# Optimization experiments

Measured on AMD Instinct MI355X. Metric: run time of the kernel, lower is better.

Reference implementation:

```python
import jax, jax.numpy as jnp
import numpy as np

B, S, D_IN, H, L = 32, 1024, 128, 256, 2
ND = 2  # bidirectional


def setup_inputs() -> dict:
    key = jax.random.key(0)
    ks = iter(jax.random.split(key, 40))

    def p(shape, scale=0.05):
        return jax.random.normal(next(ks), shape, dtype=jnp.float32) * scale

    inp = {"x": jax.random.normal(next(ks), (B, S, D_IN), dtype=jnp.float32)}
    dims_in = [D_IN, H * ND]
    for l in range(L):
        for tag in ("f", "b"):
            inp[f"w_ih_l{l}{tag}"] = p((4 * H, dims_in[l]))
            inp[f"w_hh_l{l}{tag}"] = p((4 * H, H))
            inp[f"b_l{l}{tag}"] = p((4 * H,))  # b_ih + b_hh fused (identical math)
    inp["attn_w"] = p((H * ND,))   # nn.Linear(2H, 1) weight
    inp["attn_b"] = p((1,))
    inp["head_w"] = p((D_IN, H * ND))  # forecasting head: Linear(2H, input_dim)
    inp["head_b"] = p((D_IN,))
    return inp


def _lstm_dir(x, w_ih, w_hh, b, reverse):
    """Single-direction LSTM over [B,S,F] -> [B,S,H]. PyTorch gate order i,f,g,o."""
    Bb = x.shape[0]
    Hh = w_hh.shape[1]
    # Precompute input projections once: [S,B,4H]
    xp = jnp.einsum('bsi,gi->sbg', x, w_ih) + b
    if reverse:
        xp = xp[::-1]
    h0 = jnp.zeros((Bb, Hh), x.dtype)
    c0 = jnp.zeros((Bb, Hh), x.dtype)

    def step(carry, gx):
        h, c = carry
        g = gx + h @ w_hh.T
        i, f, gg, o = jnp.split(g, 4, axis=-1)
        c = jax.nn.sigmoid(f) * c + jax.nn.sigmoid(i) * jnp.tanh(gg)
        h = jax.nn.sigmoid(o) * jnp.tanh(c)
        return (h, c), h

    _, hs = jax.lax.scan(step, (h0, c0), xp)
    if reverse:
        hs = hs[::-1]
    return jnp.swapaxes(hs, 0, 1)  # [B,S,H]


def reference(x,
              w_ih_l0f, w_hh_l0f, b_l0f, w_ih_l0b, w_hh_l0b, b_l0b,
              w_ih_l1f, w_hh_l1f, b_l1f, w_ih_l1b, w_hh_l1b, b_l1b,
              attn_w, attn_b, head_w, head_b):
    h = x
    layers = [((w_ih_l0f, w_hh_l0f, b_l0f), (w_ih_l0b, w_hh_l0b, b_l0b)),
              ((w_ih_l1f, w_hh_l1f, b_l1f), (w_ih_l1b, w_hh_l1b, b_l1b))]
    for fw, bw in layers:
        hf = _lstm_dir(h, *fw, False)
        hb = _lstm_dir(h, *bw, True)
        h = jnp.concatenate([hf, hb], axis=-1)  # [B,S,2H]; dropout off (eval)
    # Prefix attention pooling: original recomputes softmax over output[:, :i+1]
    # for every i. Equivalently (softmax is shift-invariant per prefix):
    # context_i = cumsum(e * h)_i / cumsum(e)_i with e = exp(s - max(s)).
    s = h @ attn_w + attn_b[0]                      # [B,S] attention scores
    e = jnp.exp(s - jnp.max(s, axis=1, keepdims=True))
    num = jnp.cumsum(e[..., None] * h, axis=1)      # [B,S,2H]
    den = jnp.cumsum(e, axis=1)[..., None]          # [B,S,1]
    context = num / den                             # [B,S,2H]
    forecasts = context @ head_w.T + head_b         # [B,S,D_IN]
    return forecasts
```

## Files before the change

### kernel.cpp

```cpp
#include <hip/hip_runtime.h>

typedef unsigned short ushort_t;
typedef unsigned int uint_t;
typedef unsigned long long u64;
typedef __attribute__((ext_vector_type(8))) short short8;
typedef __attribute__((ext_vector_type(4))) float floatx4;

#define S_LEN 1024
#define BATCH 32
#define HDIM  256
#define GDIM  1024
#define DIN   128
#define SALT  0x00C0FFEE00000000ULL

__device__ __forceinline__ float bf2f(ushort_t u) { return __uint_as_float(((unsigned)u) << 16); }
__device__ __forceinline__ float bf2fs(short s)   { return __uint_as_float(((unsigned)(unsigned short)s) << 16); }
__device__ __forceinline__ ushort_t f2bf(float f) {
  unsigned u = __float_as_uint(f);
  unsigned r = (u + 0x7fffu + ((u >> 16) & 1u)) >> 16;
  return (ushort_t)r;
}
__device__ __forceinline__ float sigf(float x) { return 1.f / (1.f + __expf(-x)); }
__device__ __forceinline__ float tanh_f(float x) {
  float ax = fabsf(x);
  float e = __expf(2.f * ax);
  float r = 1.f - 2.f / (e + 1.f);
  return x < 0.f ? -r : r;
}

__device__ __forceinline__ void load_lds16(const void* g, void* l) {
  __builtin_amdgcn_global_load_lds((const __attribute__((address_space(1))) unsigned int*)g,
                                   (__attribute__((address_space(3))) unsigned int*)l, 16, 0, 0);
}
__device__ __forceinline__ void vm0() { asm volatile("s_waitcnt vmcnt(0)" ::: "memory"); }

__global__ __launch_bounds__(256) void gemm_bf16(
    const ushort_t* __restrict__ A, const ushort_t* __restrict__ Bw,
    const float* __restrict__ bias, void* __restrict__ Cout,
    int M, int N, int K, int mode)
{
  __shared__ __align__(16) ushort_t As[128 * 64];
  __shared__ __align__(16) ushort_t Bs[128 * 64];
  const int tid = threadIdx.x;
  const int lane = tid & 63, wid = tid >> 6;
  const int wm = wid >> 1, wn = wid & 1;
  const int bm = blockIdx.y, bn = blockIdx.x;
  const int l15 = lane & 15, q4 = lane >> 4;

  const int r  = tid >> 3;
  const int c8 = tid & 7;
  const int g8 = c8 ^ (r & 7);

  floatx4 zero4 = {0.f, 0.f, 0.f, 0.f};
  floatx4 acc[4][4];
#pragma unroll
  for (int mt = 0; mt < 4; ++mt)
#pragma unroll
    for (int nt = 0; nt < 4; ++nt) acc[mt][nt] = zero4;

  for (int k0 = 0; k0 < K; k0 += 64) {
    __syncthreads();
#pragma unroll
    for (int p = 0; p < 4; ++p) {
      int row = p * 32 + r;
      load_lds16(A + (size_t)(bm * 128 + row) * K + k0 + g8 * 8, (void*)(As + p * 2048 + wid * 512));
      load_lds16(Bw + (size_t)(bn * 128 + row) * K + k0 + g8 * 8, (void*)(Bs + p * 2048 + wid * 512));
    }
    __syncthreads();
#pragma unroll
    for (int ks = 0; ks < 2; ++ks) {
      const int kk = ks * 4 + q4;
      short8 af[4], bf[4];
#pragma unroll
      for (int mt = 0; mt < 4; ++mt) {
        int row = wm * 64 + mt * 16 + l15;
        af[mt] = *(const short8*)(As + row * 64 + ((kk ^ (row & 7)) << 3));
      }
#pragma unroll
      for (int nt = 0; nt < 4; ++nt) {
        int row = wn * 64 + nt * 16 + l15;
        bf[nt] = *(const short8*)(Bs + row * 64 + ((kk ^ (row & 7)) << 3));
      }
#pragma unroll
      for (int mt = 0; mt < 4; ++mt)
#pragma unroll
        for (int nt = 0; nt < 4; ++nt)
          acc[mt][nt] = __builtin_amdgcn_mfma_f32_16x16x32_bf16(af[mt], bf[nt], acc[mt][nt], 0, 0, 0);
    }
  }

#pragma unroll
  for (int mt = 0; mt < 4; ++mt)
#pragma unroll
    for (int nt = 0; nt < 4; ++nt)
#pragma unroll
      for (int rr = 0; rr < 4; ++rr) {
        int m = bm * 128 + wm * 64 + mt * 16 + q4 * 4 + rr;
        int n = bn * 128 + wn * 64 + nt * 16 + l15;
        float v = acc[mt][nt][rr] + bias[n];
        if (mode == 0) {
          ((ushort_t*)Cout)[(size_t)m * N + n] = f2bf(v);
        } else if (mode == 1) {
          int t = m >> 5, b = m & 31;
          ((float*)Cout)[(size_t)b * (S_LEN * DIN) + t * DIN + n] = v;
        } else {
          int t = m >> 5, b = m & 31;
          ((ushort_t*)Cout)[(size_t)t * (N * 32) + n * 32 + b] = f2bf(v);
        }
      }
}

__global__ __launch_bounds__(256) void lstm_layer(
    const ushort_t* __restrict__ xpf, const ushort_t* __restrict__ xpb,
    const ushort_t* __restrict__ whhf, const ushort_t* __restrict__ whhb,
    ushort_t* __restrict__ hout, u64* __restrict__ comm, u64* __restrict__ epochs)
{
  const int bx = blockIdx.x;
  const int dir = bx & 1, j = bx >> 1;

  const ushort_t* xp  = dir ? xpb : xpf;
  const ushort_t* whh = dir ? whhb : whhf;
  u64* commd = comm + (size_t)dir * 4096;
  const int hoff = dir * 256;

  __shared__ __align__(16) ushort_t hbuf[32 * 264];
  __shared__ __align__(16) float stage[32 * 132];

  const int tid = threadIdx.x, lane = tid & 63, w = tid >> 6;
  const int l15 = lane & 15, q4 = lane >> 4;

  short8 Bf[2][8];
#pragma unroll
  for (int tl = 0; tl < 2; ++tl) {
    int grow = w * 256 + j * 32 + tl * 16 + l15;
#pragma unroll
    for (int ks = 0; ks < 8; ++ks)
      Bf[tl][ks] = *(const short8*)(whh + (size_t)grow * 256 + ks * 32 + q4 * 8);
  }

  for (int i = tid; i < 32 * 132; i += 256) ((uint_t*)hbuf)[i] = 0u;

  float cst[4] = {0.f, 0.f, 0.f, 0.f};

  u64 xr64[2][2];
  auto ldxp = [&](int tt) {
#pragma unroll
    for (int mt = 0; mt < 2; ++mt)
#pragma unroll
      for (int tl = 0; tl < 2; ++tl) {
        int g = w * 256 + j * 32 + tl * 16 + l15;
        xr64[mt][tl] = *(const u64*)(xp + (size_t)tt * (GDIM * BATCH) + (size_t)g * 32 + mt * 16 + q4 * 4);
      }
  };

  const int cb  = tid >> 3;
  const int cg0 = tid & 7;
  const int bb  = tid >> 3;
  const int c4  = (tid & 7) * 4;

  ldxp((dir == 0) ? 0 : 1023);
  __syncthreads();

  for (int sc = 0; sc < 1024; ++sc) {
    const int tcur  = (dir == 0) ? sc : 1023 - sc;
    const int tnext = (dir == 0) ? (sc < 1023 ? sc + 1 : 1023) : (sc < 1023 ? 1022 - sc : 0);

    floatx4 acc[2][2];
#pragma unroll
    for (int mt = 0; mt < 2; ++mt)
#pragma unroll
      for (int tl = 0; tl < 2; ++tl) {
        u64 v = xr64[mt][tl];
#pragma unroll
        for (int rr = 0; rr < 4; ++rr)
          acc[mt][tl][rr] = bf2f((ushort_t)(v >> (16 * rr)));
      }

    ldxp(tnext);

    if (sc > 0) {
      if (w == 0) {
        const u64 want = SALT | (u64)(unsigned)sc;
        const u64* ea = epochs + ((size_t)(dir * 2 + (sc & 1)) * 8 + (lane & 7)) * 16;
        for (;;) {
          u64 v = __hip_atomic_load(ea, __ATOMIC_RELAXED, __HIP_MEMORY_SCOPE_AGENT);
          if (__ballot(v == want) == ~0ULL) break;
        }
      }
      __syncthreads();
      const u64* rbuf = commd + (size_t)(sc & 1) * 2048 + (size_t)cb * 64 + cg0 * 8;
      u64 tmp[8];
#pragma unroll
      for (int k = 0; k < 8; ++k)
        tmp[k] = __hip_atomic_load(rbuf + k, __ATOMIC_RELAXED, __HIP_MEMORY_SCOPE_AGENT);
#pragma unroll
      for (int k = 0; k < 8; ++k)
        *(u64*)(hbuf + cb * 264 + cg0 * 32 + k * 4) = tmp[k];
    }
    __syncthreads();

#pragma unroll
    for (int ks = 0; ks < 8; ++ks) {
      short8 a0 = *(const short8*)(hbuf + l15 * 264 + ks * 32 + q4 * 8);
      short8 a1 = *(const short8*)(hbuf + (16 + l15) * 264 + ks * 32 + q4 * 8);
      acc[0][0] = __builtin_amdgcn_mfma_f32_16x16x32_bf16(a0, Bf[0][ks], acc[0][0], 0, 0, 0);
      acc[0][1] = __builtin_amdgcn_mfma_f32_16x16x32_bf16(a0, Bf[1][ks], acc[0][1], 0, 0, 0);
      acc[1][0] = __builtin_amdgcn_mfma_f32_16x16x32_bf16(a1, Bf[0][ks], acc[1][0], 0, 0, 0);
      acc[1][1] = __builtin_amdgcn_mfma_f32_16x16x32_bf16(a1, Bf[1][ks], acc[1][1], 0, 0, 0);
    }

#pragma unroll
    for (int mt = 0; mt < 2; ++mt)
#pragma unroll
      for (int tl = 0; tl < 2; ++tl)
#pragma unroll
        for (int rr = 0; rr < 4; ++rr)
          stage[(mt * 16 + q4 * 4 + rr) * 132 + w * 32 + tl * 16 + l15] = acc[mt][tl][rr];
    __syncthreads();

    float hv4[4];
#pragma unroll
    for (int i = 0; i < 4; ++i) {
      float gi = stage[bb * 132 +       c4 + i];
      float gf = stage[bb * 132 + 32  + c4 + i];
      float gg = stage[bb * 132 + 64  + c4 + i];
      float go = stage[bb * 132 + 96  + c4 + i];
      float c = sigf(gf) * cst[i] + sigf(gi) * tanh_f(gg);
      cst[i] = c;
      hv4[i] = sigf(go) * tanh_f(c);
    }
    u64 pv = (u64)f2bf(hv4[0]) | ((u64)f2bf(hv4[1]) << 16) |
             ((u64)f2bf(hv4[2]) << 32) | ((u64)f2bf(hv4[3]) << 48);

    __hip_atomic_store(commd + (size_t)((sc + 1) & 1) * 2048 + (size_t)bb * 64 + j * 8 + (tid & 7),
                       pv, __ATOMIC_RELAXED, __HIP_MEMORY_SCOPE_AGENT);
    *(u64*)(hout + (size_t)tcur * (BATCH * 512) + bb * 512 + hoff + j * 32 + c4) = pv;
    vm0();
    __syncthreads();
    if (tid == 0)
      __hip_atomic_store(epochs + ((size_t)(dir * 2 + ((sc + 1) & 1)) * 8 + j) * 16,
                         SALT | (u64)(unsigned)(sc + 1), __ATOMIC_RELAXED, __HIP_MEMORY_SCOPE_AGENT);
  }
}

__global__ __launch_bounds__(256) void attn_scores(
    const ushort_t* __restrict__ h1, const float* __restrict__ attn_w,
    const float* __restrict__ attn_b, float* __restrict__ e_out)
{
  const int b = blockIdx.x;
  __shared__ float sbuf[1024];
  __shared__ float red[4];
  const int tid = threadIdx.x, lane = tid & 63, w = tid >> 6;

  float wreg[8];
#pragma unroll
  for (int i = 0; i < 8; ++i) wreg[i] = attn_w[lane * 8 + i];

  for (int t = w; t < 1024; t += 4) {
    short8 hv = *(const short8*)(h1 + (size_t)t * (BATCH * 512) + b * 512 + lane * 8);
    float dot = 0.f;
#pragma unroll
    for (int i = 0; i < 8; ++i) dot += bf2fs(hv[i]) * wreg[i];
#pragma unroll
    for (int off = 32; off; off >>= 1) dot += __shfl_xor(dot, off);
    if (lane == 0) sbuf[t] = dot + attn_b[0];
  }
  __syncthreads();
  float m = -1e30f;
  for (int t = tid; t < 1024; t += 256) m = fmaxf(m, sbuf[t]);
#pragma unroll
  for (int off = 32; off; off >>= 1) m = fmaxf(m, __shfl_xor(m, off));
  if (lane == 0) red[w] = m;
  __syncthreads();
  float mm = fmaxf(fmaxf(red[0], red[1]), fmaxf(red[2], red[3]));
  for (int t = tid; t < 1024; t += 256) e_out[b * 1024 + t] = __expf(sbuf[t] - mm);
}

__global__ __launch_bounds__(256) void attn_ctx(
    const ushort_t* __restrict__ h1, const float* __restrict__ e_in, ushort_t* __restrict__ ctx)
{
  const int b = blockIdx.x >> 1, half = blockIdx.x & 1;
  const int c = half * 256 + threadIdx.x;
  float num = 0.f, den = 0.f;
  const ushort_t* hp = h1 + b * 512 + c;
  ushort_t* cp = ctx + b * 512 + c;
  const float* ep = e_in + b * 1024;
#pragma unroll 4
  for (int t = 0; t < 1024; ++t) {
    float ev = ep[t];
    float hv = bf2f(hp[(size_t)t * (BATCH * 512)]);
    num += ev * hv;
    den += ev;
    cp[(size_t)t * (BATCH * 512)] = f2bf(num / den);
  }
}

__global__ void castw(const float* __restrict__ in, ushort_t* __restrict__ out, int n) {
  int i = blockIdx.x * 256 + threadIdx.x;
  if (i < n) out[i] = f2bf(in[i]);
}
__global__ void castx(const float* __restrict__ x, ushort_t* __restrict__ xt) {
  int i = blockIdx.x * 256 + threadIdx.x;
  int dcol = i & 127;
  int m = i >> 7;
  int b = m & 31, s = m >> 5;
  xt[i] = f2bf(x[(size_t)b * (S_LEN * DIN) + s * DIN + dcol]);
}

extern "C" void kernel_launch(void* const* d_in, const int* in_sizes, int n_in,
                              void* d_out, int out_size, void* d_ws, size_t ws_size,
                              hipStream_t stream)
{
  const float* x     = (const float*)d_in[0];
  const float* wih0f = (const float*)d_in[1];
  const float* whh0f = (const float*)d_in[2];
  const float* b0f   = (const float*)d_in[3];
  const float* wih0b = (const float*)d_in[4];
  const float* whh0b = (const float*)d_in[5];
  const float* b0b   = (const float*)d_in[6];
  const float* wih1f = (const float*)d_in[7];
  const float* whh1f = (const float*)d_in[8];
  const float* b1f   = (const float*)d_in[9];
  const float* wih1b = (const float*)d_in[10];
  const float* whh1b = (const float*)d_in[11];
  const float* b1b   = (const float*)d_in[12];
  const float* attw  = (const float*)d_in[13];
  const float* attb  = (const float*)d_in[14];
  const float* headw = (const float*)d_in[15];
  const float* headb = (const float*)d_in[16];
  float* out = (float*)d_out;

  char* p = (char*)d_ws;
  auto alloc = [&](size_t bytes) {
    char* r = p;
    p += (bytes + 511) & ~(size_t)511;
    return r;
  };
  u64* ep0        = (u64*)alloc(512 * 8);
  u64* ep1        = (u64*)alloc(512 * 8);
  u64* comm0      = (u64*)alloc(8192 * 8);
  u64* comm1      = (u64*)alloc(8192 * 8);
  ushort_t* xt    = (ushort_t*)alloc((size_t)32768 * 128 * 2);
  ushort_t* cwih0f = (ushort_t*)alloc(131072 * 2);
  ushort_t* cwih0b = (ushort_t*)alloc(131072 * 2);
  ushort_t* cwhh0f = (ushort_t*)alloc(262144 * 2);
  ushort_t* cwhh0b = (ushort_t*)alloc(262144 * 2);
  ushort_t* cwih1f = (ushort_t*)alloc(524288 * 2);
  ushort_t* cwih1b = (ushort_t*)alloc(524288 * 2);
  ushort_t* cwhh1f = (ushort_t*)alloc(262144 * 2);
  ushort_t* cwhh1b = (ushort_t*)alloc(262144 * 2);
  ushort_t* cwhead = (ushort_t*)alloc(65536 * 2);
  ushort_t* xpA = (ushort_t*)alloc((size_t)32768 * 1024 * 2);
  ushort_t* xpB = (ushort_t*)alloc((size_t)32768 * 1024 * 2);
  ushort_t* h0  = (ushort_t*)alloc((size_t)32768 * 512 * 2);
  ushort_t* h1  = (ushort_t*)alloc((size_t)32768 * 512 * 2);
  float* ebuf   = (float*)alloc(32 * 1024 * 4);
  ushort_t* ctx = xpA;

  (void)in_sizes; (void)n_in; (void)out_size; (void)ws_size;

  (void)hipMemsetAsync(ep0, 0, 2 * 512 * 8, stream);

  castw<<<512, 256, 0, stream>>>(wih0f, cwih0f, 131072);
  castw<<<512, 256, 0, stream>>>(wih0b, cwih0b, 131072);
  castw<<<1024, 256, 0, stream>>>(whh0f, cwhh0f, 262144);
  castw<<<1024, 256, 0, stream>>>(whh0b, cwhh0b, 262144);
  castw<<<2048, 256, 0, stream>>>(wih1f, cwih1f, 524288);
  castw<<<2048, 256, 0, stream>>>(wih1b, cwih1b, 524288);
  castw<<<1024, 256, 0, stream>>>(whh1f, cwhh1f, 262144);
  castw<<<1024, 256, 0, stream>>>(whh1b, cwhh1b, 262144);
  castw<<<256, 256, 0, stream>>>(headw, cwhead, 65536);
  castx<<<16384, 256, 0, stream>>>(x, xt);

  gemm_bf16<<<dim3(8, 256), 256, 0, stream>>>(xt, cwih0f, b0f, xpA, 32768, 1024, 128, 2);
  gemm_bf16<<<dim3(8, 256), 256, 0, stream>>>(xt, cwih0b, b0b, xpB, 32768, 1024, 128, 2);
  lstm_layer<<<16, 256, 0, stream>>>(xpA, xpB, cwhh0f, cwhh0b, h0, comm0, ep0);

  gemm_bf16<<<dim3(8, 256), 256, 0, stream>>>(h0, cwih1f, b1f, xpA, 32768, 1024, 512, 2);
  gemm_bf16<<<dim3(8, 256), 256, 0, stream>>>(h0, cwih1b, b1b, xpB, 32768, 1024, 512, 2);
  lstm_layer<<<16, 256, 0, stream>>>(xpA, xpB, cwhh1f, cwhh1b, h1, comm1, ep1);

  attn_scores<<<32, 256, 0, stream>>>(h1, attw, attb, ebuf);
  attn_ctx<<<64, 256, 0, stream>>>(h1, ebuf, ctx);
  gemm_bf16<<<dim3(1, 256), 256, 0, stream>>>(ctx, cwhead, headb, out, 32768, 128, 512, 1);
}
```

Baseline: 7.826 ms.

## Replace epoch flags with per-element tagged hidden-state exchange in LSTM recurrence

```diff
diff --git a/kernel.cpp b/kernel.cpp
--- a/kernel.cpp
+++ b/kernel.cpp
@@ -11,7 +11,6 @@
 #define HDIM  256
 #define GDIM  1024
 #define DIN   128
-#define SALT  0x00C0FFEE00000000ULL
 
 __device__ __forceinline__ float bf2f(ushort_t u) { return __uint_as_float(((unsigned)u) << 16); }
 __device__ __forceinline__ float bf2fs(short s)   { return __uint_as_float(((unsigned)(unsigned short)s) << 16); }
@@ -32,7 +31,6 @@
   __builtin_amdgcn_global_load_lds((const __attribute__((address_space(1))) unsigned int*)g,
                                    (__attribute__((address_space(3))) unsigned int*)l, 16, 0, 0);
 }
-__device__ __forceinline__ void vm0() { asm volatile("s_waitcnt vmcnt(0)" ::: "memory"); }
 
 __global__ __launch_bounds__(256) void gemm_bf16(
     const ushort_t* __restrict__ A, const ushort_t* __restrict__ Bw,
@@ -113,18 +111,18 @@
 __global__ __launch_bounds__(256) void lstm_layer(
     const ushort_t* __restrict__ xpf, const ushort_t* __restrict__ xpb,
     const ushort_t* __restrict__ whhf, const ushort_t* __restrict__ whhb,
-    ushort_t* __restrict__ hout, u64* __restrict__ comm, u64* __restrict__ epochs)
+    ushort_t* __restrict__ hout, uint_t* __restrict__ comm)
 {
   const int bx = blockIdx.x;
   const int dir = bx & 1, j = bx >> 1;
 
   const ushort_t* xp  = dir ? xpb : xpf;
   const ushort_t* whh = dir ? whhb : whhf;
-  u64* commd = comm + (size_t)dir * 4096;
+  uint_t* commd = comm + (size_t)dir * 16384;
   const int hoff = dir * 256;
 
   __shared__ __align__(16) ushort_t hbuf[32 * 264];
-  __shared__ __align__(16) float stage[32 * 132];
+  __shared__ __align__(16) float stage[32 * 133];
 
   const int tid = threadIdx.x, lane = tid & 63, w = tid >> 6;
   const int l15 = lane & 15, q4 = lane >> 4;
@@ -155,7 +153,6 @@
 
   const int cb  = tid >> 3;
   const int cg0 = tid & 7;
-  const int bb  = tid >> 3;
   const int c4  = (tid & 7) * 4;
 
   ldxp((dir == 0) ? 0 : 1023);
@@ -178,24 +175,29 @@
 
     ldxp(tnext);
 
-    if (sc > 0) {
-      if (w == 0) {
-        const u64 want = SALT | (u64)(unsigned)sc;
-        const u64* ea = epochs + ((size_t)(dir * 2 + (sc & 1)) * 8 + (lane & 7)) * 16;
-        for (;;) {
-          u64 v = __hip_atomic_load(ea, __ATOMIC_RELAXED, __HIP_MEMORY_SCOPE_AGENT);
-          if (__ballot(v == want) == ~0ULL) break;
+    if (sc > 0 && cg0 != j) {
+      const u64* rbuf = (const u64*)(commd + (size_t)(sc & 1) * 8192 + cb * 256 + cg0 * 32);
+      const uint_t want = (uint_t)sc;
+      u64 wv[16];
+      for (;;) {
+        uint_t bad = 0;
+#pragma unroll
+        for (int k = 0; k < 16; ++k)
+          wv[k] = __hip_atomic_load(rbuf + k, __ATOMIC_RELAXED, __HIP_MEMORY_SCOPE_AGENT);
+#pragma unroll
+        for (int k = 0; k < 16; ++k) {
+          bad |= ((uint_t)wv[k] ^ want);
+          bad |= ((uint_t)(wv[k] >> 32) ^ want);
         }
-      }
-      __syncthreads();
-      const u64* rbuf = commd + (size_t)(sc & 1) * 2048 + (size_t)cb * 64 + cg0 * 8;
-      u64 tmp[8];
-#pragma unroll
-      for (int k = 0; k < 8; ++k)
-        tmp[k] = __hip_atomic_load(rbuf + k, __ATOMIC_RELAXED, __HIP_MEMORY_SCOPE_AGENT);
-#pragma unroll
-      for (int k = 0; k < 8; ++k)
-        *(u64*)(hbuf + cb * 264 + cg0 * 32 + k * 4) = tmp[k];
+        if (!(bad & 0xFFFFu)) break;
+      }
+#pragma unroll
+      for (int k = 0; k < 8; ++k) {
+        u64 a = wv[2 * k], b = wv[2 * k + 1];
+        uint_t p01 = (((uint_t)(a >> 16)) & 0xFFFFu) | (((uint_t)(a >> 32)) & 0xFFFF0000u);
+        uint_t p23 = (((uint_t)(b >> 16)) & 0xFFFFu) | (((uint_t)(b >> 32)) & 0xFFFF0000u);
+        *(u64*)(hbuf + cb * 264 + cg0 * 32 + k * 4) = (u64)p01 | ((u64)p23 << 32);
+      }
     }
     __syncthreads();
 
@@ -215,31 +217,33 @@
       for (int tl = 0; tl < 2; ++tl)
 #pragma unroll
         for (int rr = 0; rr < 4; ++rr)
-          stage[(mt * 16 + q4 * 4 + rr) * 132 + w * 32 + tl * 16 + l15] = acc[mt][tl][rr];
+          stage[(mt * 16 + q4 * 4 + rr) * 133 + w * 32 + tl * 16 + l15] = acc[mt][tl][rr];
     __syncthreads();
 
     float hv4[4];
+    ushort_t hb[4];
 #pragma unroll
     for (int i = 0; i < 4; ++i) {
-      float gi = stage[bb * 132 +       c4 + i];
-      float gf = stage[bb * 132 + 32  + c4 + i];
-      float gg = stage[bb * 132 + 64  + c4 + i];
-      float go = stage[bb * 132 + 96  + c4 + i];
+      float gi = stage[cb * 133 +      c4 + i];
+      float gf = stage[cb * 133 + 32 + c4 + i];
+      float gg = stage[cb * 133 + 64 + c4 + i];
+      float go = stage[cb * 133 + 96 + c4 + i];
       float c = sigf(gf) * cst[i] + sigf(gi) * tanh_f(gg);
       cst[i] = c;
       hv4[i] = sigf(go) * tanh_f(c);
-    }
-    u64 pv = (u64)f2bf(hv4[0]) | ((u64)f2bf(hv4[1]) << 16) |
-             ((u64)f2bf(hv4[2]) << 32) | ((u64)f2bf(hv4[3]) << 48);
-
-    __hip_atomic_store(commd + (size_t)((sc + 1) & 1) * 2048 + (size_t)bb * 64 + j * 8 + (tid & 7),
-                       pv, __ATOMIC_RELAXED, __HIP_MEMORY_SCOPE_AGENT);
-    *(u64*)(hout + (size_t)tcur * (BATCH * 512) + bb * 512 + hoff + j * 32 + c4) = pv;
-    vm0();
-    __syncthreads();
-    if (tid == 0)
-      __hip_atomic_store(epochs + ((size_t)(dir * 2 + ((sc + 1) & 1)) * 8 + j) * 16,
-                         SALT | (u64)(unsigned)(sc + 1), __ATOMIC_RELAXED, __HIP_MEMORY_SCOPE_AGENT);
+      hb[i] = f2bf(hv4[i]);
+    }
+    u64 pv = (u64)hb[0] | ((u64)hb[1] << 16) | ((u64)hb[2] << 32) | ((u64)hb[3] << 48);
+
+    const uint_t tagv = (uint_t)(sc + 1);
+    u64 w0 = ((u64)((((uint_t)hb[0]) << 16) | tagv)) | (((u64)((((uint_t)hb[1]) << 16) | tagv)) << 32);
+    u64 w1 = ((u64)((((uint_t)hb[2]) << 16) | tagv)) | (((u64)((((uint_t)hb[3]) << 16) | tagv)) << 32);
+    u64* cd = (u64*)(commd + (size_t)((sc + 1) & 1) * 8192 + cb * 256 + j * 32 + c4);
+    __hip_atomic_store(cd,     w0, __ATOMIC_RELAXED, __HIP_MEMORY_SCOPE_AGENT);
+    __hip_atomic_store(cd + 1, w1, __ATOMIC_RELAXED, __HIP_MEMORY_SCOPE_AGENT);
+
+    *(u64*)(hbuf + cb * 264 + j * 32 + c4) = pv;
+    *(u64*)(hout + (size_t)tcur * (BATCH * 512) + cb * 512 + hoff + j * 32 + c4) = pv;
   }
 }
 
@@ -336,10 +340,8 @@
     p += (bytes + 511) & ~(size_t)511;
     return r;
   };
-  u64* ep0        = (u64*)alloc(512 * 8);
-  u64* ep1        = (u64*)alloc(512 * 8);
-  u64* comm0      = (u64*)alloc(8192 * 8);
-  u64* comm1      = (u64*)alloc(8192 * 8);
+  uint_t* comm0t  = (uint_t*)alloc(32768 * 4);
+  uint_t* comm1t  = (uint_t*)alloc(32768 * 4);
   ushort_t* xt    = (ushort_t*)alloc((size_t)32768 * 128 * 2);
   ushort_t* cwih0f = (ushort_t*)alloc(131072 * 2);
   ushort_t* cwih0b = (ushort_t*)alloc(131072 * 2);
@@ -359,7 +361,7 @@
 
   (void)in_sizes; (void)n_in; (void)out_size; (void)ws_size;
 
-  (void)hipMemsetAsync(ep0, 0, 2 * 512 * 8, stream);
+  (void)hipMemsetAsync(comm0t, 0, 2 * 32768 * 4, stream);
 
   castw<<<512, 256, 0, stream>>>(wih0f, cwih0f, 131072);
   castw<<<512, 256, 0, stream>>>(wih0b, cwih0b, 131072);
@@ -374,11 +376,11 @@
 
   gemm_bf16<<<dim3(8, 256), 256, 0, stream>>>(xt, cwih0f, b0f, xpA, 32768, 1024, 128, 2);
   gemm_bf16<<<dim3(8, 256), 256, 0, stream>>>(xt, cwih0b, b0b, xpB, 32768, 1024, 128, 2);
-  lstm_layer<<<16, 256, 0, stream>>>(xpA, xpB, cwhh0f, cwhh0b, h0, comm0, ep0);
+  lstm_layer<<<16, 256, 0, stream>>>(xpA, xpB, cwhh0f, cwhh0b, h0, comm0t);
 
   gemm_bf16<<<dim3(8, 256), 256, 0, stream>>>(h0, cwih1f, b1f, xpA, 32768, 1024, 512, 2);
   gemm_bf16<<<dim3(8, 256), 256, 0, stream>>>(h0, cwih1b, b1b, xpB, 32768, 1024, 512, 2);
-  lstm_layer<<<16, 256, 0, stream>>>(xpA, xpB, cwhh1f, cwhh1b, h1, comm1, ep1);
+  lstm_layer<<<16, 256, 0, stream>>>(xpA, xpB, cwhh1f, cwhh1b, h1, comm1t);
 
   attn_scores<<<32, 256, 0, stream>>>(h1, attw, attb, ebuf);
   attn_ctx<<<64, 256, 0, stream>>>(h1, ebuf, ctx);
```

Measured after the change: 9.371 ms. 19.7% more time.

## Streamline LSTM per-step inter-block sync and skip reloading own hidden slice

Applied to the files above, without the earlier changes.

```diff
diff --git a/kernel.cpp b/kernel.cpp
--- a/kernel.cpp
+++ b/kernel.cpp
@@ -11,7 +11,6 @@
 #define HDIM  256
 #define GDIM  1024
 #define DIN   128
-#define SALT  0x00C0FFEE00000000ULL
 
 __device__ __forceinline__ float bf2f(ushort_t u) { return __uint_as_float(((unsigned)u) << 16); }
 __device__ __forceinline__ float bf2fs(short s)   { return __uint_as_float(((unsigned)(unsigned short)s) << 16); }
@@ -33,6 +32,13 @@
                                    (__attribute__((address_space(3))) unsigned int*)l, 16, 0, 0);
 }
 __device__ __forceinline__ void vm0() { asm volatile("s_waitcnt vmcnt(0)" ::: "memory"); }
+
+__device__ __forceinline__ void lds_barrier() {
+  __builtin_amdgcn_sched_barrier(0);
+  asm volatile("s_waitcnt lgkmcnt(0)" ::: "memory");
+  __builtin_amdgcn_s_barrier();
+  __builtin_amdgcn_sched_barrier(0);
+}
 
 __global__ __launch_bounds__(256) void gemm_bf16(
     const ushort_t* __restrict__ A, const ushort_t* __restrict__ Bw,
@@ -124,7 +130,7 @@
   const int hoff = dir * 256;
 
   __shared__ __align__(16) ushort_t hbuf[32 * 264];
-  __shared__ __align__(16) float stage[32 * 132];
+  __shared__ __align__(16) float stage[32 * 133];
 
   const int tid = threadIdx.x, lane = tid & 63, w = tid >> 6;
   const int l15 = lane & 15, q4 = lane >> 4;
@@ -155,7 +161,6 @@
 
   const int cb  = tid >> 3;
   const int cg0 = tid & 7;
-  const int bb  = tid >> 3;
   const int c4  = (tid & 7) * 4;
 
   ldxp((dir == 0) ? 0 : 1023);
@@ -179,25 +184,25 @@
     ldxp(tnext);
 
     if (sc > 0) {
-      if (w == 0) {
-        const u64 want = SALT | (u64)(unsigned)sc;
-        const u64* ea = epochs + ((size_t)(dir * 2 + (sc & 1)) * 8 + (lane & 7)) * 16;
-        for (;;) {
-          u64 v = __hip_atomic_load(ea, __ATOMIC_RELAXED, __HIP_MEMORY_SCOPE_AGENT);
-          if (__ballot(v == want) == ~0ULL) break;
-        }
-      }
-      __syncthreads();
-      const u64* rbuf = commd + (size_t)(sc & 1) * 2048 + (size_t)cb * 64 + cg0 * 8;
-      u64 tmp[8];
-#pragma unroll
-      for (int k = 0; k < 8; ++k)
-        tmp[k] = __hip_atomic_load(rbuf + k, __ATOMIC_RELAXED, __HIP_MEMORY_SCOPE_AGENT);
-#pragma unroll
-      for (int k = 0; k < 8; ++k)
-        *(u64*)(hbuf + cb * 264 + cg0 * 32 + k * 4) = tmp[k];
-    }
-    __syncthreads();
+      const u64 want = (u64)(unsigned)sc;
+      const u64* ea = epochs + ((size_t)(dir * 2 + (sc & 1)) * 8 + (lane & 7)) * 16;
+      for (;;) {
+        u64 v = (lane < 8) ? __hip_atomic_load(ea, __ATOMIC_RELAXED, __HIP_MEMORY_SCOPE_AGENT)
+                           : want;
+        if (__ballot(v >= want) == ~0ULL) break;
+      }
+      if (cg0 != j) {
+        const u64* rbuf = commd + (size_t)(sc & 1) * 2048 + (size_t)cb * 64 + cg0 * 8;
+        u64 tmp[8];
+#pragma unroll
+        for (int k = 0; k < 8; ++k)
+          tmp[k] = __hip_atomic_load(rbuf + k, __ATOMIC_RELAXED, __HIP_MEMORY_SCOPE_AGENT);
+#pragma unroll
+        for (int k = 0; k < 8; ++k)
+          *(u64*)(hbuf + cb * 264 + cg0 * 32 + k * 4) = tmp[k];
+      }
+    }
+    lds_barrier();
 
 #pragma unroll
     for (int ks = 0; ks < 8; ++ks) {
@@ -215,16 +220,16 @@
       for (int tl = 0; tl < 2; ++tl)
 #pragma unroll
         for (int rr = 0; rr < 4; ++rr)
-          stage[(mt * 16 + q4 * 4 + rr) * 132 + w * 32 + tl * 16 + l15] = acc[mt][tl][rr];
-    __syncthreads();
+          stage[(mt * 16 + q4 * 4 + rr) * 133 + w * 32 + tl * 16 + l15] = acc[mt][tl][rr];
+    lds_barrier();
 
     float hv4[4];
 #pragma unroll
     for (int i = 0; i < 4; ++i) {
-      float gi = stage[bb * 132 +       c4 + i];
-      float gf = stage[bb * 132 + 32  + c4 + i];
-      float gg = stage[bb * 132 + 64  + c4 + i];
-      float go = stage[bb * 132 + 96  + c4 + i];
+      float gi = stage[cb * 133 +      c4 + i];
+      float gf = stage[cb * 133 + 32 + c4 + i];
+      float gg = stage[cb * 133 + 64 + c4 + i];
+      float go = stage[cb * 133 + 96 + c4 + i];
       float c = sigf(gf) * cst[i] + sigf(gi) * tanh_f(gg);
       cst[i] = c;
       hv4[i] = sigf(go) * tanh_f(c);
@@ -232,14 +237,18 @@
     u64 pv = (u64)f2bf(hv4[0]) | ((u64)f2bf(hv4[1]) << 16) |
              ((u64)f2bf(hv4[2]) << 32) | ((u64)f2bf(hv4[3]) << 48);
 
-    __hip_atomic_store(commd + (size_t)((sc + 1) & 1) * 2048 + (size_t)bb * 64 + j * 8 + (tid & 7),
+    __hip_atomic_store(commd + (size_t)((sc + 1) & 1) * 2048 + (size_t)cb * 64 + j * 8 + (tid & 7),
                        pv, __ATOMIC_RELAXED, __HIP_MEMORY_SCOPE_AGENT);
-    *(u64*)(hout + (size_t)tcur * (BATCH * 512) + bb * 512 + hoff + j * 32 + c4) = pv;
+    *(u64*)(hbuf + cb * 264 + j * 32 + c4) = pv;
     vm0();
-    __syncthreads();
+    __builtin_amdgcn_sched_barrier(0);
+    __builtin_amdgcn_s_barrier();
+    __builtin_amdgcn_sched_barrier(0);
     if (tid == 0)
       __hip_atomic_store(epochs + ((size_t)(dir * 2 + ((sc + 1) & 1)) * 8 + j) * 16,
-                         SALT | (u64)(unsigned)(sc + 1), __ATOMIC_RELAXED, __HIP_MEMORY_SCOPE_AGENT);
+                         (u64)(unsigned)(sc + 1), __ATOMIC_RELAXED, __HIP_MEMORY_SCOPE_AGENT);
+
+    *(u64*)(hout + (size_t)tcur * (BATCH * 512) + cb * 512 + hoff + j * 32 + c4) = pv;
   }
 }
 
```

After: 7.595 ms. 3.0% less time.
